# Kernel tuning notes

Hardware: AMD Instinct MI355X
Metric: run time of the kernel (lower is better)

The kernel has to match this reference:

```python
import jax, jax.numpy as jnp
import numpy as np

LOG2 = float(np.log(2.0))
INV_SQRT3 = float(1.0 / np.sqrt(3.0))

def ssp(x):
    # ShiftedSoftPlus: softplus(x) - log(2)
    return jax.nn.softplus(x) - LOG2

def setup_inputs() -> dict:
    key = jax.random.key(0)
    ks = jax.random.split(key, 13)
    N, E, M, A, R, H = 50000, 800000, 32, 16, 8, 64
    return {
        "node_feats": jax.random.normal(ks[0], (N, 4 * M), dtype=jnp.float32),  # 32x0e + 32x1o flat
        "node_attrs": jax.random.normal(ks[1], (N, A), dtype=jnp.float32),
        "edge_embedding": jax.random.uniform(ks[2], (E, R), dtype=jnp.float32),  # radial basis, 0e
        "edge_attrs": jax.random.normal(ks[3], (E, 4), dtype=jnp.float32),  # SH: 1x0e + 1x1o
        "edge_index": jax.random.randint(ks[4], (2, E), 0, N),
        "W1s": jax.random.normal(ks[5], (M, M), dtype=jnp.float32),
        "W1v": jax.random.normal(ks[6], (M, M), dtype=jnp.float32),
        "Wr0": jax.random.normal(ks[7], (R, H), dtype=jnp.float32),
        "Wr1": jax.random.normal(ks[8], (H, 4 * M), dtype=jnp.float32),  # tp.weight_numel = 4 paths * 32 mul
        "W2s": jax.random.normal(ks[9], (2 * M, M), dtype=jnp.float32),
        "W2v": jax.random.normal(ks[10], (2 * M, M), dtype=jnp.float32),
        "Wsc_s": jax.random.normal(ks[11], (M, A, M), dtype=jnp.float32),
        "Wsc_v": jax.random.normal(ks[12], (M, A, M), dtype=jnp.float32),
    }

def reference(node_feats, node_attrs, edge_embedding, edge_attrs, edge_index,
              W1s, W1v, Wr0, Wr1, W2s, W2v, Wsc_s, Wsc_v):
    N = node_feats.shape[0]
    M = 32           # multiplicity of each irrep
    A = node_attrs.shape[1]
    AVG_NEIGH = 16.0
    # split flat irreps features: [N,32] scalars (0e), [N,32,3] vectors (1o)
    s_in = node_feats[:, :M]
    v_in = node_feats[:, M:].reshape(N, M, 3)

    # linear_1: per-irrep channel mixing, e3nn 1/sqrt(fan_in) normalization
    inv_m = 1.0 / float(np.sqrt(M))
    s = (s_in @ W1s) * inv_m                                  # [N,32]
    v = jnp.einsum('nmc,mk->nkc', v_in, W1v) * inv_m          # [N,32,3]

    # radial MLP on edge scalars -> per-edge tensor-product path weights [E,4,32]
    h = ssp((edge_embedding @ Wr0) * (1.0 / float(np.sqrt(edge_embedding.shape[1]))))
    w = (h @ Wr1) * (1.0 / float(np.sqrt(h.shape[1])))
    w = w.reshape(-1, 4, M)
    w0, w1, w2, w3 = w[:, 0], w[:, 1], w[:, 2], w[:, 3]

    src, dst = edge_index[0], edge_index[1]
    ss = s[src]                                               # [E,32]
    vv = v[src]                                               # [E,32,3]
    e0 = edge_attrs[:, :1]                                    # [E,1]  Y_0
    e1 = edge_attrs[:, 1:4]                                   # [E,3]  Y_1

    # weighted CG tensor product, 'uvu' paths (component normalization)
    m0 = w0 * ss * e0                                                   # 0e x 0e -> 0e
    m3 = w3 * jnp.einsum('emc,ec->em', vv, e1) * INV_SQRT3              # 1o x 1o -> 0e
    m1 = w1[:, :, None] * ss[:, :, None] * e1[:, None, :]               # 0e x 1o -> 1o
    m2 = w2[:, :, None] * vv * e0[:, :, None]                           # 1o x 0e -> 1o
    mid_s = jnp.concatenate([m0, m3], axis=1)                           # [E,64]
    mid_v = jnp.concatenate([m1, m2], axis=1)                           # [E,64,3]

    # scatter-sum to destination nodes
    ns = jax.ops.segment_sum(mid_s, dst, num_segments=N)
    nv = jax.ops.segment_sum(mid_v, dst, num_segments=N)
    neigh = 1.0 / float(np.sqrt(AVG_NEIGH))

    # linear_2 on simplified mid irreps 64x0e + 64x1o
    inv2 = 1.0 / float(np.sqrt(2 * M))
    out_s = (ns @ W2s) * (inv2 * neigh)
    out_v = jnp.einsum('nmc,mk->nkc', nv, W2v) * (inv2 * neigh)

    # self connection: FullyConnectedTensorProduct(node_feats_in, node_attrs)
    fc = 1.0 / float(np.sqrt(M * A))
    out_s = out_s + jnp.einsum('nu,na,uaw->nw', s_in, node_attrs, Wsc_s) * fc
    out_v = out_v + jnp.einsum('nuc,na,uaw->nwc', v_in, node_attrs, Wsc_v) * fc

    return jnp.concatenate([out_s, out_v.reshape(N, 3 * M)], axis=1)
```

## Files before the change

kernel.cpp:

```cpp
#include <hip/hip_runtime.h>
#include <stdint.h>
#include <math.h>

typedef __attribute__((ext_vector_type(8))) short bf16x8;
typedef __attribute__((ext_vector_type(4))) float f32x4;

__device__ __forceinline__ unsigned short f2bf(float f){
  unsigned int u = __float_as_uint(f);
  u += 0x7fffu + ((u >> 16) & 1u);
  return (unsigned short)(u >> 16);
}

__device__ __forceinline__ float bf2f(short s){
  return __uint_as_float(((unsigned int)(unsigned short)s) << 16);
}

__device__ __forceinline__ float ssp_f(float x){
  float u = exp2f(-fabsf(x)*1.4426950408889634f);
  return fmaxf(x, 0.f) + 0.6931471805599453f*(__log2f(1.0f + u) - 1.0f);
}

__global__ void k_count(const int* __restrict__ eidx, int E, int* __restrict__ cnt){
  int e = blockIdx.x*256 + threadIdx.x;
  if(e < E) atomicAdd(&cnt[eidx[E + e]], 1);
}

__global__ void k_scan_a(const int* __restrict__ cnt, int N, int* __restrict__ offs, int* __restrict__ bsum){
  __shared__ int arr[1024];
  int t = threadIdx.x, i = blockIdx.x*1024 + t;
  int v = (i < N) ? cnt[i] : 0;
  int own = v;
  arr[t] = v;
  for(int off = 1; off < 1024; off <<= 1){
    __syncthreads();
    int u = (t >= off) ? arr[t - off] : 0;
    __syncthreads();
    arr[t] += u;
  }
  if(i < N) offs[i] = arr[t] - own;
  if(t == 1023) bsum[blockIdx.x] = arr[1023];
}

__global__ void k_scan_b(int* __restrict__ bsum, int NB, int* __restrict__ offs, int N){
  if(threadIdx.x == 0 && blockIdx.x == 0){
    int run = 0;
    for(int b = 0; b < NB; b++){ int t = bsum[b]; bsum[b] = run; run += t; }
    offs[N] = run;
  }
}

__global__ void k_scan_c(int* __restrict__ offs, const int* __restrict__ bsum, int* __restrict__ cursor, int N){
  int i = blockIdx.x*1024 + threadIdx.x;
  if(i < N){
    int v = offs[i] + bsum[blockIdx.x];
    offs[i] = v;
    cursor[i] = v;
  }
}

__global__ void k_scatter(const int* __restrict__ eidx, int E, int* __restrict__ cursor, int* __restrict__ eid){
  int e = blockIdx.x*256 + threadIdx.x;
  if(e < E){
    int d = eidx[E + e];
    int p = atomicAdd(&cursor[d], 1);
    eid[p] = e;
  }
}

__global__ void k_prepw(const float* __restrict__ Wr0, const float* __restrict__ Wr1,
                        unsigned short* __restrict__ wr1frag, float* __restrict__ wr0p){
  int id = blockIdx.x*256 + threadIdx.x;
  if(id < 512) wr0p[id] = Wr0[(id & 7)*64 + (id >> 3)];
  if(id < 1024){
    int fi = id >> 6, lane = id & 63;
    int c0 = lane & 15, g = lane >> 4;
    int kt = fi >> 3, ct = fi & 7;
    unsigned short tmp[8];
    #pragma unroll
    for(int i = 0; i < 8; i++){
      int k = kt*32 + g*8 + i;
      tmp[i] = f2bf(Wr1[k*128 + ct*16 + c0]);
    }
    #pragma unroll
    for(int i = 0; i < 8; i++) wr1frag[id*8 + i] = tmp[i];
  }
}

__global__ __launch_bounds__(256) void k_node(
    const float* __restrict__ nf, const float* __restrict__ na,
    const float* __restrict__ W1s, const float* __restrict__ W1v,
    const float* __restrict__ Wsc_s, const float* __restrict__ Wsc_v,
    unsigned short* __restrict__ sv, float* __restrict__ out, int N)
{
  __shared__ float xl[64*133];
  __shared__ float al[64*20];
  const int t = threadIdx.x;
  const int n0 = blockIdx.x*64;

  for(int idx = t; idx < 64*128; idx += 256){
    int r = idx >> 7, c = idx & 127;
    int n = n0 + r;
    xl[r*133 + c] = (n < N) ? nf[(size_t)n*128 + c] : 0.f;
  }
  for(int idx = t; idx < 64*16; idx += 256){
    int r = idx >> 4, c = idx & 15;
    int n = n0 + r;
    al[r*20 + c] = (n < N) ? na[(size_t)n*16 + c] : 0.f;
  }
  __syncthreads();

  const float INVM = 0.17677669529663689f;
  const float FC   = 0.044194173824159216f;

  {
    int node = t & 63;
    int wvq  = t >> 6;
    if(n0 + node < N){
      unsigned short* svr = sv + (size_t)(n0+node)*128;
      for(int j = 0; j < 8; j++){
        int q  = wvq + 4*j;
        int k0 = q*4;
        float a0=0.f, a1=0.f, a2=0.f, a3=0.f;
        if(k0 < 32){
          for(int m = 0; m < 32; m++){
            float xv = xl[node*133 + m];
            f32x4 w4 = *(const f32x4*)&W1s[m*32 + k0];
            a0 += xv*w4[0]; a1 += xv*w4[1]; a2 += xv*w4[2]; a3 += xv*w4[3];
          }
        } else {
          int cc = (k0-32) >> 5, kk = (k0-32) & 31;
          for(int m = 0; m < 32; m++){
            float xv = xl[node*133 + 32 + 3*m + cc];
            f32x4 w4 = *(const f32x4*)&W1v[m*32 + kk];
            a0 += xv*w4[0]; a1 += xv*w4[1]; a2 += xv*w4[2]; a3 += xv*w4[3];
          }
        }
        int q16 = k0 >> 4;
        int cb  = k0 & 15;
        svr[(cb+0)*8 + q16] = f2bf(a0*INVM);
        svr[(cb+1)*8 + q16] = f2bf(a1*INVM);
        svr[(cb+2)*8 + q16] = f2bf(a2*INVM);
        svr[(cb+3)*8 + q16] = f2bf(a3*INVM);
      }
    }
  }

  const int lane = t & 63, wv = t >> 6;
  const int c0 = lane & 15, g = lane >> 4;
  const float* Wsc = (wv == 0) ? Wsc_s : Wsc_v;

  f32x4 accm[4][2];
  #pragma unroll
  for(int rt = 0; rt < 4; rt++)
    #pragma unroll
    for(int ct = 0; ct < 2; ct++) accm[rt][ct] = (f32x4){0.f,0.f,0.f,0.f};

  for(int ks = 0; ks < 16; ks++){
    bf16x8 bfr[2];
    #pragma unroll
    for(int ct = 0; ct < 2; ct++){
      bf16x8 b;
      #pragma unroll
      for(int i = 0; i < 8; i++){
        int k = ks*32 + g*8 + i;
        int col = ct*16 + c0;
        b[i] = (short)f2bf(Wsc[k*32 + col]);
      }
      bfr[ct] = b;
    }
    int u2 = ks*2 + (g >> 1);
    int ab = (g & 1)*8;
    #pragma unroll
    for(int rt = 0; rt < 4; rt++){
      int row = rt*16 + c0;
      float xv = (wv == 0) ? xl[row*133 + u2] : xl[row*133 + 32 + 3*u2 + (wv-1)];
      bf16x8 a;
      #pragma unroll
      for(int i = 0; i < 8; i++) a[i] = (short)f2bf(xv * al[row*20 + ab + i]);
      #pragma unroll
      for(int ct = 0; ct < 2; ct++)
        accm[rt][ct] = __builtin_amdgcn_mfma_f32_16x16x32_bf16(a, bfr[ct], accm[rt][ct], 0, 0, 0);
    }
  }

  #pragma unroll
  for(int rt = 0; rt < 4; rt++)
    #pragma unroll
    for(int ct = 0; ct < 2; ct++)
      #pragma unroll
      for(int i = 0; i < 4; i++){
        int node = n0 + rt*16 + g*4 + i;
        if(node < N){
          int col = ct*16 + c0;
          float v = accm[rt][ct][i] * FC;
          if(wv == 0) out[(size_t)node*128 + col] = v;
          else        out[(size_t)node*128 + 32 + 3*col + (wv-1)] = v;
        }
      }
}

__global__ __launch_bounds__(256, 4) void k_wedge(
    const float* __restrict__ eemb, const float* __restrict__ eattr,
    const int* __restrict__ eidx, const int* __restrict__ eid,
    const unsigned short* __restrict__ wr1frag, const float* __restrict__ wr0p,
    unsigned short* __restrict__ wper, float* __restrict__ eattr_perm,
    int* __restrict__ src_perm, int NB16, int E)
{
  __shared__ __align__(16) float wr0t[512];
  __shared__ __align__(16) unsigned short bwl[8192];
  const int t = threadIdx.x;
  {
    const f32x4* s4 = (const f32x4*)wr1frag;
    f32x4* d4 = (f32x4*)bwl;
    #pragma unroll
    for(int i = 0; i < 4; i++) d4[t + i*256] = s4[t + i*256];
    if(t < 128) ((f32x4*)wr0t)[t] = ((const f32x4*)wr0p)[t];
  }
  __syncthreads();

  const int lane = t & 63;
  const int wv   = t >> 6;
  const int c0   = lane & 15;
  const int g    = lane >> 4;
  const float S8 = 0.35355339059327373f;

  int p = blockIdx.x*4 + wv;
  if(p >= NB16) return;
  int p16 = p*16;
  int bc = E - p16; if(bc > 16) bc = 16;
  bool val = (c0 < bc);

  int e = eid[p16 + (val ? c0 : 0)];

  if(g == 0 && val){
    src_perm[p16 + c0] = eidx[e];
    *(f32x4*)(eattr_perm + (size_t)(p16 + c0)*4) = *(const f32x4*)(eattr + (size_t)e*4);
  }

  f32x4 p0 = *(const f32x4*)(eemb + (size_t)e*8);
  f32x4 p1 = *(const f32x4*)(eemb + (size_t)e*8 + 4);
  float ee[8];
  ee[0]=p0[0]; ee[1]=p0[1]; ee[2]=p0[2]; ee[3]=p0[3];
  ee[4]=p1[0]; ee[5]=p1[1]; ee[6]=p1[2]; ee[7]=p1[3];

  bf16x8 afr[2];
  #pragma unroll
  for(int kt = 0; kt < 2; kt++){
    bf16x8 a;
    #pragma unroll
    for(int i = 0; i < 8; i++){
      int j = kt*32 + g*8 + i;
      f32x4 wa = *(const f32x4*)&wr0t[j*8];
      f32x4 wb = *(const f32x4*)&wr0t[j*8 + 4];
      float pre = ee[0]*wa[0] + ee[1]*wa[1] + ee[2]*wa[2] + ee[3]*wa[3]
                + ee[4]*wb[0] + ee[5]*wb[1] + ee[6]*wb[2] + ee[7]*wb[3];
      a[i] = (short)f2bf(ssp_f(pre * S8));
    }
    afr[kt] = a;
  }

  f32x4 cfr[8];
  #pragma unroll
  for(int ct = 0; ct < 8; ct++) cfr[ct] = (f32x4){0.f,0.f,0.f,0.f};
  #pragma unroll
  for(int kt = 0; kt < 2; kt++)
    #pragma unroll
    for(int ct = 0; ct < 8; ct++){
      bf16x8 bfr = *(const bf16x8*)&bwl[((kt*8 + ct)*64 + lane)*8];
      cfr[ct] = __builtin_amdgcn_mfma_f32_16x16x32_bf16(afr[kt], bfr, cfr[ct], 0, 0, 0);
    }

  #pragma unroll
  for(int i = 0; i < 4; i++){
    if(g*4 + i < bc){
      bf16x8 wpk;
      #pragma unroll
      for(int ct = 0; ct < 8; ct++) wpk[ct] = (short)f2bf(cfr[ct][i] * 0.125f);
      *(bf16x8*)(wper + (size_t)(p16 + g*4 + i)*128 + c0*8) = wpk;
    }
  }
}

__global__ __launch_bounds__(256, 4) void k_msg(
    const unsigned short* __restrict__ sv, const unsigned short* __restrict__ wper,
    const float* __restrict__ eattr_perm, const int* __restrict__ src_perm,
    const int* __restrict__ offs, const float* __restrict__ W2s,
    const float* __restrict__ W2v, float* __restrict__ out, int N)
{
  __shared__ __align__(16) float nsl[4][256];
  __shared__ __align__(16) float w2sT[32*68];
  __shared__ __align__(16) float w2vT[32*68];
  const int t = threadIdx.x, lane = t & 63, wv = t >> 6;
  const int c0 = lane & 15, g = lane >> 4;

  {
    #pragma unroll
    for(int i = 0; i < 8; i++){
      int idx = t + i*256;
      int m = idx >> 5, o = idx & 31;
      w2sT[o*68 + m] = W2s[idx];
      w2vT[o*68 + m] = W2v[idx];
    }
  }
  __syncthreads();

  const int n = blockIdx.x*4 + wv;
  if(n >= N) return;

  const float SC2 = 0.03125f;
  const float IS3 = 0.57735026918962576f;

  float acc[16];
  #pragma unroll
  for(int i = 0; i < 16; i++) acc[i] = 0.f;

  const int eb0 = offs[n], eb1 = offs[n+1];
  for(int eb = eb0; eb < eb1; eb += 16){
    int bc = eb1 - eb; if(bc > 16) bc = 16;
    #pragma unroll
    for(int r = 0; r < 4; r++){
      int es = r*4 + g;
      if(es >= bc) continue;
      int e = eb + es;
      int s = src_perm[e];
      bf16x8 sr = *(const bf16x8*)(sv + (size_t)s*128 + c0*8);
      f32x4 ea = *(const f32x4*)(eattr_perm + (size_t)e*4);
      bf16x8 w8 = *(const bf16x8*)(wper + (size_t)e*128 + c0*8);
      float w0A = bf2f(w8[0]), w0B = bf2f(w8[1]);
      float w1A = bf2f(w8[2]), w1B = bf2f(w8[3]);
      float w2A = bf2f(w8[4]), w2B = bf2f(w8[5]);
      float w3A = bf2f(w8[6]), w3B = bf2f(w8[7]);
      float ssA = bf2f(sr[0]), ssB = bf2f(sr[1]);
      float vA0 = bf2f(sr[2]), vB0 = bf2f(sr[3]);
      float vA1 = bf2f(sr[4]), vB1 = bf2f(sr[5]);
      float vA2 = bf2f(sr[6]), vB2 = bf2f(sr[7]);
      float e0 = ea[0], e1x = ea[1], e1y = ea[2], e1z = ea[3];

      acc[0] += w0A*ssA*e0;
      acc[1] += w0B*ssB*e0;
      acc[2] += w3A*(vA0*e1x + vA1*e1y + vA2*e1z);
      acc[3] += w3B*(vB0*e1x + vB1*e1y + vB2*e1z);
      float h1A = w1A*ssA, h1B = w1B*ssB;
      acc[4]  += h1A*e1x; acc[5]  += h1A*e1y; acc[6]  += h1A*e1z;
      acc[7]  += h1B*e1x; acc[8]  += h1B*e1y; acc[9]  += h1B*e1z;
      float h2A = w2A*e0, h2B = w2B*e0;
      acc[10] += h2A*vA0; acc[11] += h2A*vA1; acc[12] += h2A*vA2;
      acc[13] += h2B*vB0; acc[14] += h2B*vB1; acc[15] += h2B*vB2;
    }
  }

  #pragma unroll
  for(int i = 0; i < 16; i++){
    acc[i] += __shfl_xor(acc[i], 16);
    acc[i] += __shfl_xor(acc[i], 32);
  }

  float* nl = nsl[wv];
  if(g == 0){
    nl[c0]      = acc[0];
    nl[16 + c0] = acc[1];
    nl[32 + c0] = acc[2]*IS3;
    nl[48 + c0] = acc[3]*IS3;
    #pragma unroll
    for(int cc = 0; cc < 3; cc++){
      nl[64 + cc*64 +  0 + c0] = acc[4  + cc];
      nl[64 + cc*64 + 16 + c0] = acc[7  + cc];
      nl[64 + cc*64 + 32 + c0] = acc[10 + cc];
      nl[64 + cc*64 + 48 + c0] = acc[13 + cc];
    }
  }
  __threadfence_block();

  const int t1 = lane, t2 = 64 + lane;
  int u1 = t1 - 32; if(u1 < 0) u1 = 0;
  const int w1i = u1/3, c1i = u1%3;
  const int w2i = (t2 - 32)/3, c2i = (t2 - 32)%3;
  const f32x4* p1a = (const f32x4*)((t1 < 32) ? &nl[0] : &nl[64 + c1i*64]);
  const f32x4* p1b = (const f32x4*)((t1 < 32) ? &w2sT[t1*68] : &w2vT[w1i*68]);
  const f32x4* p2a = (const f32x4*)&nl[64 + c2i*64];
  const f32x4* p2b = (const f32x4*)&w2vT[w2i*68];
  float s1 = 0.f, s2 = 0.f;
  #pragma unroll
  for(int q = 0; q < 16; q++){
    f32x4 a = p1a[q], b = p1b[q];
    f32x4 c = p2a[q], d = p2b[q];
    s1 += a[0]*b[0] + a[1]*b[1] + a[2]*b[2] + a[3]*b[3];
    s2 += c[0]*d[0] + c[1]*d[1] + c[2]*d[2] + c[3]*d[3];
  }
  out[(size_t)n*128 + t1] += s1*SC2;
  out[(size_t)n*128 + t2] += s2*SC2;
}

extern "C" void kernel_launch(void* const* d_in, const int* in_sizes, int n_in,
                              void* d_out, int out_size, void* d_ws, size_t ws_size,
                              hipStream_t stream)
{
  const float* nf    = (const float*)d_in[0];
  const float* na    = (const float*)d_in[1];
  const float* eemb  = (const float*)d_in[2];
  const float* eattr = (const float*)d_in[3];
  const int*   eidx  = (const int*)d_in[4];
  const float* W1s   = (const float*)d_in[5];
  const float* W1v   = (const float*)d_in[6];
  const float* Wr0   = (const float*)d_in[7];
  const float* Wr1   = (const float*)d_in[8];
  const float* W2s   = (const float*)d_in[9];
  const float* W2v   = (const float*)d_in[10];
  const float* Wsc_s = (const float*)d_in[11];
  const float* Wsc_v = (const float*)d_in[12];
  float* out = (float*)d_out;

  int N = in_sizes[0]/128;
  int E = in_sizes[2]/8;
  int NB16 = (E + 15)/16;

  char* ws = (char*)d_ws;
  size_t off = 0;
  unsigned short* sv = (unsigned short*)(ws + off); off += (size_t)N*128*2;
  unsigned short* wper = (unsigned short*)(ws + off); off += (size_t)NB16*16*128*2;
  float* eattr_perm = (float*)(ws + off);     off += (size_t)NB16*16*4*4;
  int* src_perm = (int*)(ws + off);           off += (size_t)NB16*16*4;
  int* cnt    = (int*)(ws + off);             off += (size_t)N*4;
  int* offs   = (int*)(ws + off);             off += (size_t)(N+1)*4;
  int* cursor = (int*)(ws + off);             off += (size_t)N*4;
  int* bsum   = (int*)(ws + off);             off += 4096;
  int* eid    = (int*)(ws + off);             off += (size_t)E*4;
  unsigned short* wr1frag = (unsigned short*)(ws + off); off += 16384;
  float* wr0p = (float*)(ws + off);           off += 2048;

  int NB = (N + 1023)/1024;

  k_prepw  <<<dim3(4),           dim3(256), 0, stream>>>(Wr0, Wr1, wr1frag, wr0p);
  (void)hipMemsetAsync(cnt, 0, (size_t)N*4, stream);
  k_count  <<<dim3((E+255)/256), dim3(256), 0, stream>>>(eidx, E, cnt);
  k_scan_a <<<dim3(NB),          dim3(1024),0, stream>>>(cnt, N, offs, bsum);
  k_scan_b <<<dim3(1),           dim3(64),  0, stream>>>(bsum, NB, offs, N);
  k_scan_c <<<dim3(NB),          dim3(1024),0, stream>>>(offs, bsum, cursor, N);
  k_scatter<<<dim3((E+255)/256), dim3(256), 0, stream>>>(eidx, E, cursor, eid);
  k_node   <<<dim3((N+63)/64),   dim3(256), 0, stream>>>(nf, na, W1s, W1v, Wsc_s, Wsc_v, sv, out, N);
  k_wedge  <<<dim3((NB16+3)/4),  dim3(256), 0, stream>>>(eemb, eattr, eidx, eid,
                                                         wr1frag, wr0p,
                                                         wper, eattr_perm, src_perm, NB16, E);
  k_msg    <<<dim3((N+3)/4),     dim3(256), 0, stream>>>(sv, wper, eattr_perm, src_perm, offs,
                                                         W2s, W2v, out, N);
}
```

Baseline: 386.3 us.

## Permute edge data in scatter pass and reduce LDS padding in linear_2

The scatter kernel now writes the source index, edge attributes and edge embedding straight to their destination-sorted positions, instead of writing an edge-id list that k_wedge then used for an indirect gather. k_wedge now reads the permuted embeddings contiguously, which drops one level of indirection and the eid buffer. The reads in the scatter become coalesced while the writes become scattered, and an extra permuted-embedding buffer is written and read back. Separately, the transposed W2 tiles in k_msg use a row stride of 66 with 2-wide vector loads instead of 68 with 4-wide loads, to change the LDS bank-conflict pattern.

```diff
diff --git a/kernel.cpp b/kernel.cpp
--- a/kernel.cpp
+++ b/kernel.cpp
@@ -4,6 +4,7 @@
 
 typedef __attribute__((ext_vector_type(8))) short bf16x8;
 typedef __attribute__((ext_vector_type(4))) float f32x4;
+typedef __attribute__((ext_vector_type(2))) float f32x2;
 
 __device__ __forceinline__ unsigned short f2bf(float f){
   unsigned int u = __float_as_uint(f);
@@ -58,12 +59,18 @@
   }
 }
 
-__global__ void k_scatter(const int* __restrict__ eidx, int E, int* __restrict__ cursor, int* __restrict__ eid){
+__global__ void k_perm(const float* __restrict__ eemb, const float* __restrict__ eattr,
+                       const int* __restrict__ eidx, int E, int* __restrict__ cursor,
+                       int* __restrict__ src_perm, float* __restrict__ eattr_perm,
+                       float* __restrict__ eemb_perm){
   int e = blockIdx.x*256 + threadIdx.x;
   if(e < E){
     int d = eidx[E + e];
-    int p = atomicAdd(&cursor[d], 1);
-    eid[p] = e;
+    int dp = atomicAdd(&cursor[d], 1);
+    src_perm[dp] = eidx[e];
+    *(f32x4*)(eattr_perm + (size_t)dp*4) = *(const f32x4*)(eattr + (size_t)e*4);
+    *(f32x4*)(eemb_perm + (size_t)dp*8)     = *(const f32x4*)(eemb + (size_t)e*8);
+    *(f32x4*)(eemb_perm + (size_t)dp*8 + 4) = *(const f32x4*)(eemb + (size_t)e*8 + 4);
   }
 }
 
@@ -200,11 +207,9 @@
 }
 
 __global__ __launch_bounds__(256, 4) void k_wedge(
-    const float* __restrict__ eemb, const float* __restrict__ eattr,
-    const int* __restrict__ eidx, const int* __restrict__ eid,
+    const float* __restrict__ eemb_perm,
     const unsigned short* __restrict__ wr1frag, const float* __restrict__ wr0p,
-    unsigned short* __restrict__ wper, float* __restrict__ eattr_perm,
-    int* __restrict__ src_perm, int NB16, int E)
+    unsigned short* __restrict__ wper, int NB16, int E)
 {
   __shared__ __align__(16) float wr0t[512];
   __shared__ __align__(16) unsigned short bwl[8192];
@@ -230,15 +235,9 @@
   int bc = E - p16; if(bc > 16) bc = 16;
   bool val = (c0 < bc);
 
-  int e = eid[p16 + (val ? c0 : 0)];
-
-  if(g == 0 && val){
-    src_perm[p16 + c0] = eidx[e];
-    *(f32x4*)(eattr_perm + (size_t)(p16 + c0)*4) = *(const f32x4*)(eattr + (size_t)e*4);
-  }
-
-  f32x4 p0 = *(const f32x4*)(eemb + (size_t)e*8);
-  f32x4 p1 = *(const f32x4*)(eemb + (size_t)e*8 + 4);
+  size_t row = (size_t)(p16 + (val ? c0 : 0))*8;
+  f32x4 p0 = *(const f32x4*)(eemb_perm + row);
+  f32x4 p1 = *(const f32x4*)(eemb_perm + row + 4);
   float ee[8];
   ee[0]=p0[0]; ee[1]=p0[1]; ee[2]=p0[2]; ee[3]=p0[3];
   ee[4]=p1[0]; ee[5]=p1[1]; ee[6]=p1[2]; ee[7]=p1[3];
@@ -288,8 +287,8 @@
     const float* __restrict__ W2v, float* __restrict__ out, int N)
 {
   __shared__ __align__(16) float nsl[4][256];
-  __shared__ __align__(16) float w2sT[32*68];
-  __shared__ __align__(16) float w2vT[32*68];
+  __shared__ __align__(8) float w2sT[32*66];
+  __shared__ __align__(8) float w2vT[32*66];
   const int t = threadIdx.x, lane = t & 63, wv = t >> 6;
   const int c0 = lane & 15, g = lane >> 4;
 
@@ -298,8 +297,8 @@
     for(int i = 0; i < 8; i++){
       int idx = t + i*256;
       int m = idx >> 5, o = idx & 31;
-      w2sT[o*68 + m] = W2s[idx];
-      w2vT[o*68 + m] = W2v[idx];
+      w2sT[o*66 + m] = W2s[idx];
+      w2vT[o*66 + m] = W2v[idx];
     }
   }
   __syncthreads();
@@ -375,17 +374,17 @@
   int u1 = t1 - 32; if(u1 < 0) u1 = 0;
   const int w1i = u1/3, c1i = u1%3;
   const int w2i = (t2 - 32)/3, c2i = (t2 - 32)%3;
-  const f32x4* p1a = (const f32x4*)((t1 < 32) ? &nl[0] : &nl[64 + c1i*64]);
-  const f32x4* p1b = (const f32x4*)((t1 < 32) ? &w2sT[t1*68] : &w2vT[w1i*68]);
-  const f32x4* p2a = (const f32x4*)&nl[64 + c2i*64];
-  const f32x4* p2b = (const f32x4*)&w2vT[w2i*68];
+  const f32x2* p1a = (const f32x2*)((t1 < 32) ? &nl[0] : &nl[64 + c1i*64]);
+  const f32x2* p1b = (const f32x2*)((t1 < 32) ? &w2sT[t1*66] : &w2vT[w1i*66]);
+  const f32x2* p2a = (const f32x2*)&nl[64 + c2i*64];
+  const f32x2* p2b = (const f32x2*)&w2vT[w2i*66];
   float s1 = 0.f, s2 = 0.f;
   #pragma unroll
-  for(int q = 0; q < 16; q++){
-    f32x4 a = p1a[q], b = p1b[q];
-    f32x4 c = p2a[q], d = p2b[q];
-    s1 += a[0]*b[0] + a[1]*b[1] + a[2]*b[2] + a[3]*b[3];
-    s2 += c[0]*d[0] + c[1]*d[1] + c[2]*d[2] + c[3]*d[3];
+  for(int q = 0; q < 32; q++){
+    f32x2 a = p1a[q], b = p1b[q];
+    f32x2 c = p2a[q], d = p2b[q];
+    s1 += a[0]*b[0] + a[1]*b[1];
+    s2 += c[0]*d[0] + c[1]*d[1];
   }
   out[(size_t)n*128 + t1] += s1*SC2;
   out[(size_t)n*128 + t2] += s2*SC2;
@@ -418,13 +417,13 @@
   size_t off = 0;
   unsigned short* sv = (unsigned short*)(ws + off); off += (size_t)N*128*2;
   unsigned short* wper = (unsigned short*)(ws + off); off += (size_t)NB16*16*128*2;
+  float* eemb_perm = (float*)(ws + off);      off += (size_t)NB16*16*8*4;
   float* eattr_perm = (float*)(ws + off);     off += (size_t)NB16*16*4*4;
   int* src_perm = (int*)(ws + off);           off += (size_t)NB16*16*4;
   int* cnt    = (int*)(ws + off);             off += (size_t)N*4;
   int* offs   = (int*)(ws + off);             off += (size_t)(N+1)*4;
   int* cursor = (int*)(ws + off);             off += (size_t)N*4;
   int* bsum   = (int*)(ws + off);             off += 4096;
-  int* eid    = (int*)(ws + off);             off += (size_t)E*4;
   unsigned short* wr1frag = (unsigned short*)(ws + off); off += 16384;
   float* wr0p = (float*)(ws + off);           off += 2048;
 
@@ -436,11 +435,10 @@
   k_scan_a <<<dim3(NB),          dim3(1024),0, stream>>>(cnt, N, offs, bsum);
   k_scan_b <<<dim3(1),           dim3(64),  0, stream>>>(bsum, NB, offs, N);
   k_scan_c <<<dim3(NB),          dim3(1024),0, stream>>>(offs, bsum, cursor, N);
-  k_scatter<<<dim3((E+255)/256), dim3(256), 0, stream>>>(eidx, E, cursor, eid);
+  k_perm   <<<dim3((E+255)/256), dim3(256), 0, stream>>>(eemb, eattr, eidx, E, cursor,
+                                                         src_perm, eattr_perm, eemb_perm);
   k_node   <<<dim3((N+63)/64),   dim3(256), 0, stream>>>(nf, na, W1s, W1v, Wsc_s, Wsc_v, sv, out, N);
-  k_wedge  <<<dim3((NB16+3)/4),  dim3(256), 0, stream>>>(eemb, eattr, eidx, eid,
-                                                         wr1frag, wr0p,
-                                                         wper, eattr_perm, src_perm, NB16, E);
+  k_wedge  <<<dim3((NB16+3)/4),  dim3(256), 0, stream>>>(eemb_perm, wr1frag, wr0p, wper, NB16, E);
   k_msg    <<<dim3((N+3)/4),     dim3(256), 0, stream>>>(sv, wper, eattr_perm, src_perm, offs,
                                                          W2s, W2v, out, N);
 }
```

Measured after the change: 388.3 us. No clear change (+0.5%).
